# Kernel tuning notes

Hardware: AMD Instinct MI355X
Metric: run time of the kernel (lower is better)

## Reference

```python
import jax, jax.numpy as jnp
import numpy as np

Q_LORA, KV_LORA = 1536, 512
NUM_HEADS, HEAD_DIM = 4, 64
B, QL, KL = 2, 4096, 4096


def setup_inputs() -> dict:
    key = jax.random.key(0)
    k1, k2, k3, k4 = jax.random.split(key, 4)
    q_compressed = jax.random.normal(k1, (B, QL, Q_LORA), dtype=jnp.float32)
    kv_compressed = jax.random.normal(k2, (B, KL, KV_LORA), dtype=jnp.float32)
    # additive causal mask: 0 on/below diagonal, -inf-like above
    causal_mask = jnp.where(
        jnp.arange(QL)[:, None] >= jnp.arange(KL)[None, :], 0.0, -1e9
    ).astype(jnp.float32)
    # learned params (Linear weights stored torch-style as [out, in])
    Wq = 0.01 * jax.random.normal(k3, (NUM_HEADS * HEAD_DIM, Q_LORA), dtype=jnp.float32)
    Wk = 0.01 * jax.random.normal(k4, (NUM_HEADS * HEAD_DIM, KV_LORA), dtype=jnp.float32)
    head_weights = jnp.ones((NUM_HEADS,), dtype=jnp.float32)
    return {
        "q_compressed": q_compressed,
        "kv_compressed": kv_compressed,
        "causal_mask": causal_mask,
        "Wq": Wq,
        "Wk": Wk,
        "head_weights": head_weights,
    }


def reference(q_compressed, kv_compressed, causal_mask, Wq, Wk, head_weights):
    b, ql, _ = q_compressed.shape
    kl = kv_compressed.shape[1]
    # projections: x @ W.T, then split heads
    q_idx = (q_compressed @ Wq.T).reshape(b, ql, NUM_HEADS, HEAD_DIM)  # [b,q,h,d]
    k_idx = (kv_compressed @ Wk.T).reshape(b, kl, NUM_HEADS, HEAD_DIM)  # [b,k,h,d]
    scores = jnp.einsum("bqhd,bkhd->bhqk", q_idx, k_idx)
    scores = jax.nn.relu(scores)
    # head-weighted sum over heads
    index_scores = jnp.einsum("bhqk,h->bqk", scores, head_weights)
    index_scores = index_scores + causal_mask[None, :, :]
    return index_scores
```

## Files before the change

### kernel.cpp

```cpp
#include <hip/hip_runtime.h>
#include <hip/hip_bf16.h>
#include <stdint.h>

typedef __attribute__((ext_vector_type(8))) short bhalf8;
typedef __attribute__((ext_vector_type(4))) float f32x4;
typedef __attribute__((ext_vector_type(4))) unsigned us4;

#define B_ 2
#define QL_ 4096
#define KL_ 4096
#define ND_ 256
#define QLORA_ 1536
#define KVLORA_ 512

__device__ __forceinline__ unsigned pack2(float lo, float hi) {
    union { float f; unsigned u; } a, b; a.f = lo; b.f = hi;
    return __builtin_amdgcn_perm(b.u, a.u, 0x07060302u);
}

__global__ __launch_bounds__(256, 4) void prep_kernel(
    const float* __restrict__ qc, const float* __restrict__ kvc,
    const float* __restrict__ Wq, const float* __restrict__ Wk,
    unsigned short* __restrict__ qidx, unsigned short* __restrict__ kidx)
{
    const int bid = blockIdx.x;
    const int tid = threadIdx.x;

    const float* A; const float* W; unsigned short* C; int K; int pb;
    if (bid < 512) { A = qc;  W = Wq; C = qidx; K = QLORA_;  pb = bid; }
    else           { A = kvc; W = Wk; C = kidx; K = KVLORA_; pb = bid - 512; }

    __shared__ unsigned short sA[2][64][72];
    __shared__ unsigned short sW[2][64][72];

    const int lane = tid & 63;
    const int wid = tid >> 6;

    const int t2 = pb >> 3;
    const int nt = t2 & 3;
    const int mt = (pb & 7) + 8 * (t2 >> 2);
    const int m0 = mt * 64, n0 = nt * 64;

    const int wm = (wid >> 1) * 32;
    const int wn = (wid & 1) * 32;

    const int sr = tid >> 3;
    const int sc = (tid & 7) * 8;

    const float* Abase = A + (size_t)(m0 + sr) * K + sc;
    const float* Wbase = W + (size_t)(n0 + sr) * K + sc;
    const size_t row32 = (size_t)32 * K;

    f32x4 pa[4], pw[4], qa[4], qw[4];
    f32x4 acc[2][2] = {};
    const int nIter = K >> 6;

    auto ISSUE = [&](int kk, f32x4* ra, f32x4* rw) {
        #pragma unroll
        for (int p = 0; p < 2; ++p) {
            ra[2 * p]     = *reinterpret_cast<const f32x4*>(Abase + row32 * p + kk);
            ra[2 * p + 1] = *reinterpret_cast<const f32x4*>(Abase + row32 * p + kk + 4);
            rw[2 * p]     = *reinterpret_cast<const f32x4*>(Wbase + row32 * p + kk);
            rw[2 * p + 1] = *reinterpret_cast<const f32x4*>(Wbase + row32 * p + kk + 4);
        }
    };
    auto WRITE = [&](int buf, f32x4* ra, f32x4* rw) {
        #pragma unroll
        for (int p = 0; p < 2; ++p) {
            us4 va = { pack2(ra[2*p][0], ra[2*p][1]), pack2(ra[2*p][2], ra[2*p][3]),
                       pack2(ra[2*p+1][0], ra[2*p+1][1]), pack2(ra[2*p+1][2], ra[2*p+1][3]) };
            *reinterpret_cast<us4*>(&sA[buf][sr + 32 * p][sc]) = va;
            us4 vw = { pack2(rw[2*p][0], rw[2*p][1]), pack2(rw[2*p][2], rw[2*p][3]),
                       pack2(rw[2*p+1][0], rw[2*p+1][1]), pack2(rw[2*p+1][2], rw[2*p+1][3]) };
            *reinterpret_cast<us4*>(&sW[buf][sr + 32 * p][sc]) = vw;
        }
    };
    auto COMPUTE = [&](int buf) {
        #pragma unroll
        for (int ks = 0; ks < 2; ++ks) {
            const int cb = ks * 32 + (lane >> 4) * 8;
            bhalf8 a0 = *reinterpret_cast<const bhalf8*>(&sA[buf][wm + (lane & 15)][cb]);
            bhalf8 a1 = *reinterpret_cast<const bhalf8*>(&sA[buf][wm + 16 + (lane & 15)][cb]);
            bhalf8 b0 = *reinterpret_cast<const bhalf8*>(&sW[buf][wn + (lane & 15)][cb]);
            bhalf8 b1 = *reinterpret_cast<const bhalf8*>(&sW[buf][wn + 16 + (lane & 15)][cb]);
            acc[0][0] = __builtin_amdgcn_mfma_f32_16x16x32_bf16(a0, b0, acc[0][0], 0, 0, 0);
            acc[0][1] = __builtin_amdgcn_mfma_f32_16x16x32_bf16(a0, b1, acc[0][1], 0, 0, 0);
            acc[1][0] = __builtin_amdgcn_mfma_f32_16x16x32_bf16(a1, b0, acc[1][0], 0, 0, 0);
            acc[1][1] = __builtin_amdgcn_mfma_f32_16x16x32_bf16(a1, b1, acc[1][1], 0, 0, 0);
        }
    };

    ISSUE(0, pa, pw);
    WRITE(0, pa, pw);
    ISSUE(64, pa, pw);
    __syncthreads();

    for (int it = 0; it < nIter; it += 2) {
        if (it + 2 < nIter) ISSUE((it + 2) << 6, qa, qw);
        COMPUTE(0);
        if (it + 1 < nIter) WRITE(1, pa, pw);
        __syncthreads();
        if (it + 3 < nIter) ISSUE((it + 3) << 6, pa, pw);
        COMPUTE(1);
        if (it + 2 < nIter) WRITE(0, qa, qw);
        __syncthreads();
    }

    #pragma unroll
    for (int i = 0; i < 2; ++i) {
        #pragma unroll
        for (int j = 0; j < 2; ++j) {
            int n = n0 + wn + j * 16 + (lane & 15);
            #pragma unroll
            for (int r = 0; r < 4; ++r) {
                int m = m0 + wm + i * 16 + (lane >> 4) * 4 + r;
                union { float f; unsigned u; } x; x.f = acc[i][j][r];
                C[(size_t)m * ND_ + n] = (unsigned short)(x.u >> 16);
            }
        }
    }
}

__global__ __launch_bounds__(512, 2) void scores_kernel(
    const unsigned short* __restrict__ Qi,
    const unsigned short* __restrict__ Ki,
    const float* __restrict__ hw,
    float* __restrict__ out)
{
    const int bx = blockIdx.x;
    const int tid = threadIdx.x;

    if (bx >= 1056) {
        int t = bx - 1056;
        int b = (t >= 496) ? 1 : 0;
        t -= b * 496;
        int tk = (int)((1.0f + __builtin_sqrtf(8.0f * (float)t + 1.0f)) * 0.5f);
        while (tk * (tk - 1) / 2 > t) --tk;
        while (tk * (tk + 1) / 2 <= t) ++tk;
        int tq = t - tk * (tk - 1) / 2;
        float* outb = out + (size_t)b * QL_ * KL_ + (size_t)tq * 128 * KL_ + tk * 128;
        const f32x4 mval = {-1e9f, -1e9f, -1e9f, -1e9f};
        #pragma unroll
        for (int p = 0; p < 8; ++p) {
            int idx = p * 512 + tid;
            int r = idx >> 5;
            int c = (idx & 31) * 4;
            *reinterpret_cast<f32x4*>(&outb[(size_t)r * KL_ + c]) = mval;
        }
        return;
    }

    int g = (bx & 7) * 132 + (bx >> 3);
    int b = (g >= 528) ? 1 : 0;
    int t = g - b * 528;
    int tq = (int)((__builtin_sqrtf(8.0f * (float)t + 1.0f) - 1.0f) * 0.5f);
    while ((tq + 1) * (tq + 2) / 2 <= t) ++tq;
    while (tq * (tq + 1) / 2 > t) --tq;
    int tk = t - tq * (tq + 1) / 2;

    const int q0 = tq * 128, k0 = tk * 128;
    float* outb = out + (size_t)b * QL_ * KL_;

    __shared__ unsigned short sQ[2][128][72];
    __shared__ unsigned short sK[2][128][72];
    const int lane = tid & 63;
    const int wid = tid >> 6;
    const int wq = (wid >> 2) * 64;
    const int wk = (wid & 3) * 32;

    const int hr = tid >> 2;
    const int hc = (tid & 3) * 16;

    float whv[4];
    #pragma unroll
    for (int h = 0; h < 4; ++h) whv[h] = hw[h];

    f32x4 oacc[4][2] = {};
    bhalf8 rq0, rq1, rk0, rk1;

    const unsigned short* Qb = Qi + (size_t)(b * QL_ + q0) * ND_;
    const unsigned short* Kb = Ki + (size_t)(b * KL_ + k0) * ND_;

    auto LOADH = [&](int h) {
        const size_t ro = (size_t)hr * ND_ + h * 64 + hc;
        rq0 = *reinterpret_cast<const bhalf8*>(&Qb[ro]);
        rq1 = *reinterpret_cast<const bhalf8*>(&Qb[ro + 8]);
        rk0 = *reinterpret_cast<const bhalf8*>(&Kb[ro]);
        rk1 = *reinterpret_cast<const bhalf8*>(&Kb[ro + 8]);
    };
    auto WRITEH = [&](int buf) {
        *reinterpret_cast<bhalf8*>(&sQ[buf][hr][hc])     = rq0;
        *reinterpret_cast<bhalf8*>(&sQ[buf][hr][hc + 8]) = rq1;
        *reinterpret_cast<bhalf8*>(&sK[buf][hr][hc])     = rk0;
        *reinterpret_cast<bhalf8*>(&sK[buf][hr][hc + 8]) = rk1;
    };
    auto COMPUTE_H = [&](int buf, int h) {
        f32x4 hacc[4][2] = {};
        #pragma unroll
        for (int ks = 0; ks < 2; ++ks) {
            const int cb = ks * 32 + (lane >> 4) * 8;
            bhalf8 bfr[2];
            #pragma unroll
            for (int j = 0; j < 2; ++j)
                bfr[j] = *reinterpret_cast<const bhalf8*>(&sK[buf][wk + j * 16 + (lane & 15)][cb]);
            #pragma unroll
            for (int i = 0; i < 4; ++i) {
                bhalf8 afr = *reinterpret_cast<const bhalf8*>(&sQ[buf][wq + i * 16 + (lane & 15)][cb]);
                #pragma unroll
                for (int j = 0; j < 2; ++j)
                    hacc[i][j] = __builtin_amdgcn_mfma_f32_16x16x32_bf16(afr, bfr[j], hacc[i][j], 0, 0, 0);
            }
        }
        const float w = whv[h];
        const f32x4 zero = {0.0f, 0.0f, 0.0f, 0.0f};
        #pragma unroll
        for (int i = 0; i < 4; ++i)
            #pragma unroll
            for (int j = 0; j < 2; ++j) {
                f32x4 m = __builtin_elementwise_max(hacc[i][j], zero);
                oacc[i][j] += w * m;
            }
    };

    LOADH(0);
    WRITEH(0);
    __syncthreads();
    #pragma unroll
    for (int h = 0; h < 4; ++h) {
        if (h < 3) LOADH(h + 1);
        COMPUTE_H(h & 1, h);
        if (h < 3) {
            WRITEH((h + 1) & 1);
            __syncthreads();
        }
    }

    const int kcb = k0 + wk + (lane & 15);
    if (tq == tk) {
        #pragma unroll
        for (int i = 0; i < 4; ++i)
            #pragma unroll
            for (int r = 0; r < 4; ++r) {
                int q = q0 + wq + i * 16 + (lane >> 4) * 4 + r;
                #pragma unroll
                for (int j = 0; j < 2; ++j) {
                    int kc = kcb + j * 16;
                    outb[(size_t)q * KL_ + kc] = oacc[i][j][r] + ((kc <= q) ? 0.0f : -1e9f);
                }
            }
    } else {
        #pragma unroll
        for (int i = 0; i < 4; ++i)
            #pragma unroll
            for (int r = 0; r < 4; ++r) {
                int q = q0 + wq + i * 16 + (lane >> 4) * 4 + r;
                #pragma unroll
                for (int j = 0; j < 2; ++j)
                    outb[(size_t)q * KL_ + kcb + j * 16] = oacc[i][j][r];
            }
    }
}

extern "C" void kernel_launch(void* const* d_in, const int* in_sizes, int n_in,
                              void* d_out, int out_size, void* d_ws, size_t ws_size,
                              hipStream_t stream) {
    const float* qc  = (const float*)d_in[0];
    const float* kvc = (const float*)d_in[1];
    const float* Wq  = (const float*)d_in[3];
    const float* Wk  = (const float*)d_in[4];
    const float* hw  = (const float*)d_in[5];

    unsigned short* qidx = (unsigned short*)d_ws;
    unsigned short* kidx = qidx + (size_t)B_ * QL_ * ND_;

    prep_kernel<<<dim3(1024), 256, 0, stream>>>(qc, kvc, Wq, Wk, qidx, kidx);
    scores_kernel<<<dim3(1056 + 992), 512, 0, stream>>>(qidx, kidx, hw, (float*)d_out);
}
```

Baseline: 60.89 us.

## Restructure projection and scores kernels for register-direct fragments and vector stores

The projection kernel now uses 128-row M tiles with half as many blocks. It loads A fragments straight from global memory into registers and converts them to bf16 in place, so only W is staged through LDS. The scores kernel loads all four heads of Q into LDS once and keeps K fragments in registers, removing the per-head syncs. It also swaps MFMA operands so the output can be written as contiguous float4 stores, and raises the occupancy hint. The aim is less LDS traffic, fewer barriers and wider stores, at the cost of uncoalesced direct global fragment loads and higher register pressure.

```diff
diff --git a/kernel.cpp b/kernel.cpp
--- a/kernel.cpp
+++ b/kernel.cpp
@@ -18,7 +18,7 @@
     return __builtin_amdgcn_perm(b.u, a.u, 0x07060302u);
 }
 
-__global__ __launch_bounds__(256, 4) void prep_kernel(
+__global__ __launch_bounds__(256, 2) void prep_kernel(
     const float* __restrict__ qc, const float* __restrict__ kvc,
     const float* __restrict__ Wq, const float* __restrict__ Wk,
     unsigned short* __restrict__ qidx, unsigned short* __restrict__ kidx)
@@ -27,101 +27,105 @@
     const int tid = threadIdx.x;
 
     const float* A; const float* W; unsigned short* C; int K; int pb;
-    if (bid < 512) { A = qc;  W = Wq; C = qidx; K = QLORA_;  pb = bid; }
-    else           { A = kvc; W = Wk; C = kidx; K = KVLORA_; pb = bid - 512; }
-
-    __shared__ unsigned short sA[2][64][72];
+    if (bid < 256) { A = qc;  W = Wq; C = qidx; K = QLORA_;  pb = bid; }
+    else           { A = kvc; W = Wk; C = kidx; K = KVLORA_; pb = bid - 256; }
+
+    const int mt = (pb & 7) + 8 * (pb >> 5);
+    const int nt = (pb >> 3) & 3;
+    const int m0 = mt * 128, n0 = nt * 64;
+
     __shared__ unsigned short sW[2][64][72];
 
     const int lane = tid & 63;
-    const int wid = tid >> 6;
-
-    const int t2 = pb >> 3;
-    const int nt = t2 & 3;
-    const int mt = (pb & 7) + 8 * (t2 >> 2);
-    const int m0 = mt * 64, n0 = nt * 64;
-
-    const int wm = (wid >> 1) * 32;
-    const int wn = (wid & 1) * 32;
-
-    const int sr = tid >> 3;
-    const int sc = (tid & 7) * 8;
-
-    const float* Abase = A + (size_t)(m0 + sr) * K + sc;
-    const float* Wbase = W + (size_t)(n0 + sr) * K + sc;
-    const size_t row32 = (size_t)32 * K;
-
-    f32x4 pa[4], pw[4], qa[4], qw[4];
-    f32x4 acc[2][2] = {};
+    const int w = tid >> 6;
+    const int l15 = lane & 15;
+    const int lh = lane >> 4;
+
+    const float* Arow0 = A + (size_t)(m0 + w * 32 + l15) * K + lh * 8;
+    const float* Arow1 = Arow0 + (size_t)16 * K;
+
+    const int wr = tid >> 2;
+    const int wc = (tid & 3) * 16;
+    const float* Wst = W + (size_t)(n0 + wr) * K + wc;
+
+    f32x4 acc[2][4] = {};
+    f32x4 pa[8], qa[8];
+    f32x4 pw[4], qw[4];
     const int nIter = K >> 6;
 
-    auto ISSUE = [&](int kk, f32x4* ra, f32x4* rw) {
-        #pragma unroll
-        for (int p = 0; p < 2; ++p) {
-            ra[2 * p]     = *reinterpret_cast<const f32x4*>(Abase + row32 * p + kk);
-            ra[2 * p + 1] = *reinterpret_cast<const f32x4*>(Abase + row32 * p + kk + 4);
-            rw[2 * p]     = *reinterpret_cast<const f32x4*>(Wbase + row32 * p + kk);
-            rw[2 * p + 1] = *reinterpret_cast<const f32x4*>(Wbase + row32 * p + kk + 4);
-        }
-    };
-    auto WRITE = [&](int buf, f32x4* ra, f32x4* rw) {
-        #pragma unroll
-        for (int p = 0; p < 2; ++p) {
-            us4 va = { pack2(ra[2*p][0], ra[2*p][1]), pack2(ra[2*p][2], ra[2*p][3]),
-                       pack2(ra[2*p+1][0], ra[2*p+1][1]), pack2(ra[2*p+1][2], ra[2*p+1][3]) };
-            *reinterpret_cast<us4*>(&sA[buf][sr + 32 * p][sc]) = va;
-            us4 vw = { pack2(rw[2*p][0], rw[2*p][1]), pack2(rw[2*p][2], rw[2*p][3]),
-                       pack2(rw[2*p+1][0], rw[2*p+1][1]), pack2(rw[2*p+1][2], rw[2*p+1][3]) };
-            *reinterpret_cast<us4*>(&sW[buf][sr + 32 * p][sc]) = vw;
-        }
-    };
-    auto COMPUTE = [&](int buf) {
+    auto ALOAD = [&](int kk, f32x4* r) {
+        #pragma unroll
+        for (int af = 0; af < 2; ++af) {
+            const float* base = (af ? Arow1 : Arow0) + kk;
+            #pragma unroll
+            for (int ks = 0; ks < 2; ++ks) {
+                r[(af * 2 + ks) * 2 + 0] = *reinterpret_cast<const f32x4*>(base + ks * 32);
+                r[(af * 2 + ks) * 2 + 1] = *reinterpret_cast<const f32x4*>(base + ks * 32 + 4);
+            }
+        }
+    };
+    auto WLOAD = [&](int kk, f32x4* r) {
+        #pragma unroll
+        for (int e = 0; e < 4; ++e)
+            r[e] = *reinterpret_cast<const f32x4*>(Wst + kk + e * 4);
+    };
+    auto WWRITE = [&](int buf, f32x4* r) {
+        us4 v0 = { pack2(r[0][0], r[0][1]), pack2(r[0][2], r[0][3]),
+                   pack2(r[1][0], r[1][1]), pack2(r[1][2], r[1][3]) };
+        us4 v1 = { pack2(r[2][0], r[2][1]), pack2(r[2][2], r[2][3]),
+                   pack2(r[3][0], r[3][1]), pack2(r[3][2], r[3][3]) };
+        *reinterpret_cast<us4*>(&sW[buf][wr][wc])     = v0;
+        *reinterpret_cast<us4*>(&sW[buf][wr][wc + 8]) = v1;
+    };
+    auto COMPUTE = [&](int buf, f32x4* ar) {
         #pragma unroll
         for (int ks = 0; ks < 2; ++ks) {
-            const int cb = ks * 32 + (lane >> 4) * 8;
-            bhalf8 a0 = *reinterpret_cast<const bhalf8*>(&sA[buf][wm + (lane & 15)][cb]);
-            bhalf8 a1 = *reinterpret_cast<const bhalf8*>(&sA[buf][wm + 16 + (lane & 15)][cb]);
-            bhalf8 b0 = *reinterpret_cast<const bhalf8*>(&sW[buf][wn + (lane & 15)][cb]);
-            bhalf8 b1 = *reinterpret_cast<const bhalf8*>(&sW[buf][wn + 16 + (lane & 15)][cb]);
-            acc[0][0] = __builtin_amdgcn_mfma_f32_16x16x32_bf16(a0, b0, acc[0][0], 0, 0, 0);
-            acc[0][1] = __builtin_amdgcn_mfma_f32_16x16x32_bf16(a0, b1, acc[0][1], 0, 0, 0);
-            acc[1][0] = __builtin_amdgcn_mfma_f32_16x16x32_bf16(a1, b0, acc[1][0], 0, 0, 0);
-            acc[1][1] = __builtin_amdgcn_mfma_f32_16x16x32_bf16(a1, b1, acc[1][1], 0, 0, 0);
-        }
-    };
-
-    ISSUE(0, pa, pw);
-    WRITE(0, pa, pw);
-    ISSUE(64, pa, pw);
+            bhalf8 bf[4];
+            #pragma unroll
+            for (int nf = 0; nf < 4; ++nf)
+                bf[nf] = *reinterpret_cast<const bhalf8*>(&sW[buf][nf * 16 + l15][ks * 32 + lh * 8]);
+            #pragma unroll
+            for (int af = 0; af < 2; ++af) {
+                f32x4* r = &ar[(af * 2 + ks) * 2];
+                us4 ap = { pack2(r[0][0], r[0][1]), pack2(r[0][2], r[0][3]),
+                           pack2(r[1][0], r[1][1]), pack2(r[1][2], r[1][3]) };
+                bhalf8 afr = *reinterpret_cast<bhalf8*>(&ap);
+                #pragma unroll
+                for (int nf = 0; nf < 4; ++nf)
+                    acc[af][nf] = __builtin_amdgcn_mfma_f32_16x16x32_bf16(bf[nf], afr, acc[af][nf], 0, 0, 0);
+            }
+        }
+    };
+
+    WLOAD(0, pw); ALOAD(0, pa);
+    WWRITE(0, pw);
     __syncthreads();
 
     for (int it = 0; it < nIter; it += 2) {
-        if (it + 2 < nIter) ISSUE((it + 2) << 6, qa, qw);
-        COMPUTE(0);
-        if (it + 1 < nIter) WRITE(1, pa, pw);
+        WLOAD((it + 1) << 6, qw); ALOAD((it + 1) << 6, qa);
+        COMPUTE(0, pa);
+        WWRITE(1, qw);
         __syncthreads();
-        if (it + 3 < nIter) ISSUE((it + 3) << 6, pa, pw);
-        COMPUTE(1);
-        if (it + 2 < nIter) WRITE(0, qa, qw);
+        if (it + 2 < nIter) { WLOAD((it + 2) << 6, pw); ALOAD((it + 2) << 6, pa); }
+        COMPUTE(1, qa);
+        if (it + 2 < nIter) WWRITE(0, pw);
         __syncthreads();
     }
 
     #pragma unroll
-    for (int i = 0; i < 2; ++i) {
-        #pragma unroll
-        for (int j = 0; j < 2; ++j) {
-            int n = n0 + wn + j * 16 + (lane & 15);
-            #pragma unroll
-            for (int r = 0; r < 4; ++r) {
-                int m = m0 + wm + i * 16 + (lane >> 4) * 4 + r;
-                union { float f; unsigned u; } x; x.f = acc[i][j][r];
-                C[(size_t)m * ND_ + n] = (unsigned short)(x.u >> 16);
-            }
-        }
-    }
-}
-
-__global__ __launch_bounds__(512, 2) void scores_kernel(
+    for (int af = 0; af < 2; ++af) {
+        const size_t mrow = (size_t)(m0 + w * 32 + af * 16 + l15) * ND_;
+        #pragma unroll
+        for (int nf = 0; nf < 4; ++nf) {
+            uint2 v;
+            v.x = pack2(acc[af][nf][0], acc[af][nf][1]);
+            v.y = pack2(acc[af][nf][2], acc[af][nf][3]);
+            *reinterpret_cast<uint2*>(&C[mrow + n0 + nf * 16 + lh * 4]) = v;
+        }
+    }
+}
+
+__global__ __launch_bounds__(512, 4) void scores_kernel(
     const unsigned short* __restrict__ Qi,
     const unsigned short* __restrict__ Ki,
     const float* __restrict__ hw,
@@ -161,103 +165,91 @@
     const int q0 = tq * 128, k0 = tk * 128;
     float* outb = out + (size_t)b * QL_ * KL_;
 
-    __shared__ unsigned short sQ[2][128][72];
-    __shared__ unsigned short sK[2][128][72];
+    __shared__ unsigned short sQ[128][264];
     const int lane = tid & 63;
     const int wid = tid >> 6;
     const int wq = (wid >> 2) * 64;
     const int wk = (wid & 3) * 32;
-
-    const int hr = tid >> 2;
-    const int hc = (tid & 3) * 16;
+    const int l15 = lane & 15;
+    const int lh = lane >> 4;
+
+    const unsigned short* Qb = Qi + (size_t)(b * QL_ + q0) * ND_;
+    const unsigned short* Kb = Ki + (size_t)(b * KL_ + k0) * ND_;
+    const unsigned short* Klane = Kb + (size_t)(wk + l15) * ND_ + lh * 8;
+
+    bhalf8 kfA[4], kfB[4];
+    auto KLOAD = [&](int h, bhalf8* kf) {
+        #pragma unroll
+        for (int j = 0; j < 2; ++j)
+            #pragma unroll
+            for (int ks = 0; ks < 2; ++ks)
+                kf[j * 2 + ks] = *reinterpret_cast<const bhalf8*>(
+                    Klane + (size_t)j * 16 * ND_ + h * 64 + ks * 32);
+    };
+
+    KLOAD(0, kfA);
+
+    {
+        const int qr = tid >> 2;
+        const int qcb = (tid & 3) * 64;
+        #pragma unroll
+        for (int p = 0; p < 8; ++p) {
+            bhalf8 v = *reinterpret_cast<const bhalf8*>(&Qb[(size_t)qr * ND_ + qcb + p * 8]);
+            *reinterpret_cast<bhalf8*>(&sQ[qr][qcb + p * 8]) = v;
+        }
+    }
+    __syncthreads();
 
     float whv[4];
     #pragma unroll
     for (int h = 0; h < 4; ++h) whv[h] = hw[h];
 
-    f32x4 oacc[4][2] = {};
-    bhalf8 rq0, rq1, rk0, rk1;
-
-    const unsigned short* Qb = Qi + (size_t)(b * QL_ + q0) * ND_;
-    const unsigned short* Kb = Ki + (size_t)(b * KL_ + k0) * ND_;
-
-    auto LOADH = [&](int h) {
-        const size_t ro = (size_t)hr * ND_ + h * 64 + hc;
-        rq0 = *reinterpret_cast<const bhalf8*>(&Qb[ro]);
-        rq1 = *reinterpret_cast<const bhalf8*>(&Qb[ro + 8]);
-        rk0 = *reinterpret_cast<const bhalf8*>(&Kb[ro]);
-        rk1 = *reinterpret_cast<const bhalf8*>(&Kb[ro + 8]);
-    };
-    auto WRITEH = [&](int buf) {
-        *reinterpret_cast<bhalf8*>(&sQ[buf][hr][hc])     = rq0;
-        *reinterpret_cast<bhalf8*>(&sQ[buf][hr][hc + 8]) = rq1;
-        *reinterpret_cast<bhalf8*>(&sK[buf][hr][hc])     = rk0;
-        *reinterpret_cast<bhalf8*>(&sK[buf][hr][hc + 8]) = rk1;
-    };
-    auto COMPUTE_H = [&](int buf, int h) {
+    f32x4 acc[4][2] = {};
+
+    auto HEAD = [&](int h, bhalf8* cur, bhalf8* nxt) {
+        if (h < 3) KLOAD(h + 1, nxt);
         f32x4 hacc[4][2] = {};
         #pragma unroll
         for (int ks = 0; ks < 2; ++ks) {
-            const int cb = ks * 32 + (lane >> 4) * 8;
-            bhalf8 bfr[2];
-            #pragma unroll
-            for (int j = 0; j < 2; ++j)
-                bfr[j] = *reinterpret_cast<const bhalf8*>(&sK[buf][wk + j * 16 + (lane & 15)][cb]);
             #pragma unroll
             for (int i = 0; i < 4; ++i) {
-                bhalf8 afr = *reinterpret_cast<const bhalf8*>(&sQ[buf][wq + i * 16 + (lane & 15)][cb]);
-                #pragma unroll
-                for (int j = 0; j < 2; ++j)
-                    hacc[i][j] = __builtin_amdgcn_mfma_f32_16x16x32_bf16(afr, bfr[j], hacc[i][j], 0, 0, 0);
-            }
-        }
-        const float w = whv[h];
+                bhalf8 qf = *reinterpret_cast<const bhalf8*>(
+                    &sQ[wq + i * 16 + l15][h * 64 + ks * 32 + lh * 8]);
+                hacc[i][0] = __builtin_amdgcn_mfma_f32_16x16x32_bf16(cur[0 * 2 + ks], qf, hacc[i][0], 0, 0, 0);
+                hacc[i][1] = __builtin_amdgcn_mfma_f32_16x16x32_bf16(cur[1 * 2 + ks], qf, hacc[i][1], 0, 0, 0);
+            }
+        }
+        const float wgt = whv[h];
         const f32x4 zero = {0.0f, 0.0f, 0.0f, 0.0f};
         #pragma unroll
         for (int i = 0; i < 4; ++i)
             #pragma unroll
             for (int j = 0; j < 2; ++j) {
                 f32x4 m = __builtin_elementwise_max(hacc[i][j], zero);
-                oacc[i][j] += w * m;
-            }
-    };
-
-    LOADH(0);
-    WRITEH(0);
-    __syncthreads();
+                acc[i][j] += wgt * m;
+            }
+    };
+
+    HEAD(0, kfA, kfB);
+    HEAD(1, kfB, kfA);
+    HEAD(2, kfA, kfB);
+    HEAD(3, kfB, kfA);
+
     #pragma unroll
-    for (int h = 0; h < 4; ++h) {
-        if (h < 3) LOADH(h + 1);
-        COMPUTE_H(h & 1, h);
-        if (h < 3) {
-            WRITEH((h + 1) & 1);
-            __syncthreads();
-        }
-    }
-
-    const int kcb = k0 + wk + (lane & 15);
-    if (tq == tk) {
-        #pragma unroll
-        for (int i = 0; i < 4; ++i)
-            #pragma unroll
-            for (int r = 0; r < 4; ++r) {
-                int q = q0 + wq + i * 16 + (lane >> 4) * 4 + r;
+    for (int i = 0; i < 4; ++i) {
+        const int q = q0 + wq + i * 16 + l15;
+        float* rowp = outb + (size_t)q * KL_;
+        #pragma unroll
+        for (int j = 0; j < 2; ++j) {
+            const int kbase = k0 + wk + j * 16 + lh * 4;
+            f32x4 v = acc[i][j];
+            if (tq == tk) {
                 #pragma unroll
-                for (int j = 0; j < 2; ++j) {
-                    int kc = kcb + j * 16;
-                    outb[(size_t)q * KL_ + kc] = oacc[i][j][r] + ((kc <= q) ? 0.0f : -1e9f);
-                }
-            }
-    } else {
-        #pragma unroll
-        for (int i = 0; i < 4; ++i)
-            #pragma unroll
-            for (int r = 0; r < 4; ++r) {
-                int q = q0 + wq + i * 16 + (lane >> 4) * 4 + r;
-                #pragma unroll
-                for (int j = 0; j < 2; ++j)
-                    outb[(size_t)q * KL_ + kcb + j * 16] = oacc[i][j][r];
-            }
+                for (int r = 0; r < 4; ++r)
+                    if (kbase + r > q) v[r] += -1e9f;
+            }
+            *reinterpret_cast<f32x4*>(&rowp[kbase]) = v;
+        }
     }
 }
 
@@ -273,6 +265,6 @@
     unsigned short* qidx = (unsigned short*)d_ws;
     unsigned short* kidx = qidx + (size_t)B_ * QL_ * ND_;
 
-    prep_kernel<<<dim3(1024), 256, 0, stream>>>(qc, kvc, Wq, Wk, qidx, kidx);
+    prep_kernel<<<dim3(512), 256, 0, stream>>>(qc, kvc, Wq, Wk, qidx, kidx);
     scores_kernel<<<dim3(1056 + 992), 512, 0, stream>>>(qidx, kidx, hw, (float*)d_out);
 }
```

Result: slower. 112.3 us (+84.4%).

## Transpose MFMA operands for vector stores, interleave fill blocks, use nontemporal writes

Applied to the files above, without the earlier changes.

Swaps the MFMA A/B operands so each lane holds four consecutive key columns of one query row. The epilogue can then emit 16-byte vector stores instead of scalar stores. Output stores, including the masked-tile fill, use nontemporal hints to avoid polluting cache with the write-only 128MB output. Block indices are remapped so compute and mask-fill blocks are interleaved in groups of 8, spreading pure-store work across the run instead of leaving it all at the tail.

```diff
diff --git a/kernel.cpp b/kernel.cpp
--- a/kernel.cpp
+++ b/kernel.cpp
@@ -16,6 +16,10 @@
 __device__ __forceinline__ unsigned pack2(float lo, float hi) {
     union { float f; unsigned u; } a, b; a.f = lo; b.f = hi;
     return __builtin_amdgcn_perm(b.u, a.u, 0x07060302u);
+}
+
+__device__ __forceinline__ void nt_store4(float* p, f32x4 v) {
+    __builtin_nontemporal_store(v, reinterpret_cast<f32x4*>(p));
 }
 
 __global__ __launch_bounds__(256, 4) void prep_kernel(
@@ -130,10 +134,18 @@
     const int bx = blockIdx.x;
     const int tid = threadIdx.x;
 
-    if (bx >= 1056) {
-        int t = bx - 1056;
-        int b = (t >= 496) ? 1 : 0;
-        t -= b * 496;
+    int c = -1, f = -1;
+    if (bx < 1984) {
+        const int seg = bx >> 4, w = bx & 15;
+        if (w < 8) c = seg * 8 + w;
+        else       f = seg * 8 + (w - 8);
+    } else {
+        c = 992 + (bx - 1984);
+    }
+
+    if (f >= 0) {
+        int b = (f >= 496) ? 1 : 0;
+        int t = f - b * 496;
         int tk = (int)((1.0f + __builtin_sqrtf(8.0f * (float)t + 1.0f)) * 0.5f);
         while (tk * (tk - 1) / 2 > t) --tk;
         while (tk * (tk + 1) / 2 <= t) ++tk;
@@ -144,13 +156,13 @@
         for (int p = 0; p < 8; ++p) {
             int idx = p * 512 + tid;
             int r = idx >> 5;
-            int c = (idx & 31) * 4;
-            *reinterpret_cast<f32x4*>(&outb[(size_t)r * KL_ + c]) = mval;
+            int cc = (idx & 31) * 4;
+            nt_store4(&outb[(size_t)r * KL_ + cc], mval);
         }
         return;
     }
 
-    int g = (bx & 7) * 132 + (bx >> 3);
+    int g = (c & 7) * 132 + (c >> 3);
     int b = (g >= 528) ? 1 : 0;
     int t = g - b * 528;
     int tq = (int)((__builtin_sqrtf(8.0f * (float)t + 1.0f) - 1.0f) * 0.5f);
@@ -167,6 +179,8 @@
     const int wid = tid >> 6;
     const int wq = (wid >> 2) * 64;
     const int wk = (wid & 3) * 32;
+    const int l15 = lane & 15;
+    const int lh = lane >> 4;
 
     const int hr = tid >> 2;
     const int hc = (tid & 3) * 16;
@@ -175,7 +189,7 @@
     #pragma unroll
     for (int h = 0; h < 4; ++h) whv[h] = hw[h];
 
-    f32x4 oacc[4][2] = {};
+    f32x4 acc[4][2] = {};
     bhalf8 rq0, rq1, rk0, rk1;
 
     const unsigned short* Qb = Qi + (size_t)(b * QL_ + q0) * ND_;
@@ -198,27 +212,27 @@
         f32x4 hacc[4][2] = {};
         #pragma unroll
         for (int ks = 0; ks < 2; ++ks) {
-            const int cb = ks * 32 + (lane >> 4) * 8;
-            bhalf8 bfr[2];
+            const int cb = ks * 32 + lh * 8;
+            bhalf8 kfr[2];
             #pragma unroll
             for (int j = 0; j < 2; ++j)
-                bfr[j] = *reinterpret_cast<const bhalf8*>(&sK[buf][wk + j * 16 + (lane & 15)][cb]);
+                kfr[j] = *reinterpret_cast<const bhalf8*>(&sK[buf][wk + j * 16 + l15][cb]);
             #pragma unroll
             for (int i = 0; i < 4; ++i) {
-                bhalf8 afr = *reinterpret_cast<const bhalf8*>(&sQ[buf][wq + i * 16 + (lane & 15)][cb]);
+                bhalf8 qfr = *reinterpret_cast<const bhalf8*>(&sQ[buf][wq + i * 16 + l15][cb]);
                 #pragma unroll
                 for (int j = 0; j < 2; ++j)
-                    hacc[i][j] = __builtin_amdgcn_mfma_f32_16x16x32_bf16(afr, bfr[j], hacc[i][j], 0, 0, 0);
-            }
-        }
-        const float w = whv[h];
+                    hacc[i][j] = __builtin_amdgcn_mfma_f32_16x16x32_bf16(kfr[j], qfr, hacc[i][j], 0, 0, 0);
+            }
+        }
+        const float wgt = whv[h];
         const f32x4 zero = {0.0f, 0.0f, 0.0f, 0.0f};
         #pragma unroll
         for (int i = 0; i < 4; ++i)
             #pragma unroll
             for (int j = 0; j < 2; ++j) {
                 f32x4 m = __builtin_elementwise_max(hacc[i][j], zero);
-                oacc[i][j] += w * m;
+                acc[i][j] += wgt * m;
             }
     };
 
@@ -235,29 +249,21 @@
         }
     }
 
-    const int kcb = k0 + wk + (lane & 15);
-    if (tq == tk) {
-        #pragma unroll
-        for (int i = 0; i < 4; ++i)
-            #pragma unroll
-            for (int r = 0; r < 4; ++r) {
-                int q = q0 + wq + i * 16 + (lane >> 4) * 4 + r;
+    #pragma unroll
+    for (int i = 0; i < 4; ++i) {
+        const int q = q0 + wq + i * 16 + l15;
+        float* rowp = outb + (size_t)q * KL_;
+        #pragma unroll
+        for (int j = 0; j < 2; ++j) {
+            const int kbase = k0 + wk + j * 16 + lh * 4;
+            f32x4 v = acc[i][j];
+            if (tq == tk) {
                 #pragma unroll
-                for (int j = 0; j < 2; ++j) {
-                    int kc = kcb + j * 16;
-                    outb[(size_t)q * KL_ + kc] = oacc[i][j][r] + ((kc <= q) ? 0.0f : -1e9f);
-                }
-            }
-    } else {
-        #pragma unroll
-        for (int i = 0; i < 4; ++i)
-            #pragma unroll
-            for (int r = 0; r < 4; ++r) {
-                int q = q0 + wq + i * 16 + (lane >> 4) * 4 + r;
-                #pragma unroll
-                for (int j = 0; j < 2; ++j)
-                    outb[(size_t)q * KL_ + kcb + j * 16] = oacc[i][j][r];
-            }
+                for (int r = 0; r < 4; ++r)
+                    if (kbase + r > q) v[r] += -1e9f;
+            }
+            nt_store4(&rowp[kbase], v);
+        }
     }
 }
 
@@ -274,5 +280,5 @@
     unsigned short* kidx = qidx + (size_t)B_ * QL_ * ND_;
 
     prep_kernel<<<dim3(1024), 256, 0, stream>>>(qc, kvc, Wq, Wk, qidx, kidx);
-    scores_kernel<<<dim3(1056 + 992), 512, 0, stream>>>(qidx, kidx, hw, (float*)d_out);
-}
+    scores_kernel<<<dim3(2048), 512, 0, stream>>>(qidx, kidx, hw, (float*)d_out);
+}
```

Result: slower. 75.28 us (+23.6%).

## Load MFMA operands directly from global memory, dropping LDS staging

Applied to the files above, without the earlier changes.

The scores kernel no longer stages Q and K head tiles through double-buffered shared memory with barriers. Each lane now loads its MFMA fragments straight from global memory, and launch bounds are raised to allow more resident blocks. This removes LDS traffic and __syncthreads, but each Q/K element is now fetched redundantly by several waves through the cache hierarchy, with no software prefetch overlap.

```diff
diff --git a/kernel.cpp b/kernel.cpp
--- a/kernel.cpp
+++ b/kernel.cpp
@@ -121,7 +121,7 @@
     }
 }
 
-__global__ __launch_bounds__(512, 2) void scores_kernel(
+__global__ __launch_bounds__(512, 4) void scores_kernel(
     const unsigned short* __restrict__ Qi,
     const unsigned short* __restrict__ Ki,
     const float* __restrict__ hw,
@@ -161,91 +161,64 @@
     const int q0 = tq * 128, k0 = tk * 128;
     float* outb = out + (size_t)b * QL_ * KL_;
 
-    __shared__ unsigned short sQ[2][128][72];
-    __shared__ unsigned short sK[2][128][72];
     const int lane = tid & 63;
     const int wid = tid >> 6;
     const int wq = (wid >> 2) * 64;
     const int wk = (wid & 3) * 32;
-
-    const int hr = tid >> 2;
-    const int hc = (tid & 3) * 16;
+    const int l15 = lane & 15;
+    const int lh = lane >> 4;
+
+    const unsigned short* Qlane = Qi + (size_t)(b * QL_ + q0 + wq + l15) * ND_ + lh * 8;
+    const unsigned short* Klane = Ki + (size_t)(b * KL_ + k0 + wk + l15) * ND_ + lh * 8;
 
     float whv[4];
     #pragma unroll
     for (int h = 0; h < 4; ++h) whv[h] = hw[h];
 
-    f32x4 oacc[4][2] = {};
-    bhalf8 rq0, rq1, rk0, rk1;
-
-    const unsigned short* Qb = Qi + (size_t)(b * QL_ + q0) * ND_;
-    const unsigned short* Kb = Ki + (size_t)(b * KL_ + k0) * ND_;
-
-    auto LOADH = [&](int h) {
-        const size_t ro = (size_t)hr * ND_ + h * 64 + hc;
-        rq0 = *reinterpret_cast<const bhalf8*>(&Qb[ro]);
-        rq1 = *reinterpret_cast<const bhalf8*>(&Qb[ro + 8]);
-        rk0 = *reinterpret_cast<const bhalf8*>(&Kb[ro]);
-        rk1 = *reinterpret_cast<const bhalf8*>(&Kb[ro + 8]);
-    };
-    auto WRITEH = [&](int buf) {
-        *reinterpret_cast<bhalf8*>(&sQ[buf][hr][hc])     = rq0;
-        *reinterpret_cast<bhalf8*>(&sQ[buf][hr][hc + 8]) = rq1;
-        *reinterpret_cast<bhalf8*>(&sK[buf][hr][hc])     = rk0;
-        *reinterpret_cast<bhalf8*>(&sK[buf][hr][hc + 8]) = rk1;
-    };
-    auto COMPUTE_H = [&](int buf, int h) {
-        f32x4 hacc[4][2] = {};
-        #pragma unroll
-        for (int ks = 0; ks < 2; ++ks) {
-            const int cb = ks * 32 + (lane >> 4) * 8;
-            bhalf8 bfr[2];
-            #pragma unroll
-            for (int j = 0; j < 2; ++j)
-                bfr[j] = *reinterpret_cast<const bhalf8*>(&sK[buf][wk + j * 16 + (lane & 15)][cb]);
-            #pragma unroll
-            for (int i = 0; i < 4; ++i) {
-                bhalf8 afr = *reinterpret_cast<const bhalf8*>(&sQ[buf][wq + i * 16 + (lane & 15)][cb]);
-                #pragma unroll
-                for (int j = 0; j < 2; ++j)
-                    hacc[i][j] = __builtin_amdgcn_mfma_f32_16x16x32_bf16(afr, bfr[j], hacc[i][j], 0, 0, 0);
-            }
-        }
-        const float w = whv[h];
-        const f32x4 zero = {0.0f, 0.0f, 0.0f, 0.0f};
-        #pragma unroll
-        for (int i = 0; i < 4; ++i)
-            #pragma unroll
-            for (int j = 0; j < 2; ++j) {
-                f32x4 m = __builtin_elementwise_max(hacc[i][j], zero);
-                oacc[i][j] += w * m;
-            }
-    };
-
-    LOADH(0);
-    WRITEH(0);
-    __syncthreads();
+    f32x4 acc[4][2] = {};
+    const f32x4 zero = {0.0f, 0.0f, 0.0f, 0.0f};
+
     #pragma unroll
     for (int h = 0; h < 4; ++h) {
-        if (h < 3) LOADH(h + 1);
-        COMPUTE_H(h & 1, h);
-        if (h < 3) {
-            WRITEH((h + 1) & 1);
-            __syncthreads();
-        }
-    }
-
-    const int kcb = k0 + wk + (lane & 15);
+        bhalf8 qf[4][2], kf[2][2];
+        #pragma unroll
+        for (int i = 0; i < 4; ++i)
+            #pragma unroll
+            for (int ks = 0; ks < 2; ++ks)
+                qf[i][ks] = *reinterpret_cast<const bhalf8*>(
+                    Qlane + (size_t)i * 16 * ND_ + h * 64 + ks * 32);
+        #pragma unroll
+        for (int j = 0; j < 2; ++j)
+            #pragma unroll
+            for (int ks = 0; ks < 2; ++ks)
+                kf[j][ks] = *reinterpret_cast<const bhalf8*>(
+                    Klane + (size_t)j * 16 * ND_ + h * 64 + ks * 32);
+
+        const float wgt = whv[h];
+        #pragma unroll
+        for (int i = 0; i < 4; ++i) {
+            #pragma unroll
+            for (int j = 0; j < 2; ++j) {
+                f32x4 hacc = zero;
+                hacc = __builtin_amdgcn_mfma_f32_16x16x32_bf16(qf[i][0], kf[j][0], hacc, 0, 0, 0);
+                hacc = __builtin_amdgcn_mfma_f32_16x16x32_bf16(qf[i][1], kf[j][1], hacc, 0, 0, 0);
+                f32x4 m = __builtin_elementwise_max(hacc, zero);
+                acc[i][j] += wgt * m;
+            }
+        }
+    }
+
+    const int kcb = k0 + wk + l15;
     if (tq == tk) {
         #pragma unroll
         for (int i = 0; i < 4; ++i)
             #pragma unroll
             for (int r = 0; r < 4; ++r) {
-                int q = q0 + wq + i * 16 + (lane >> 4) * 4 + r;
+                int q = q0 + wq + i * 16 + lh * 4 + r;
                 #pragma unroll
                 for (int j = 0; j < 2; ++j) {
                     int kc = kcb + j * 16;
-                    outb[(size_t)q * KL_ + kc] = oacc[i][j][r] + ((kc <= q) ? 0.0f : -1e9f);
+                    outb[(size_t)q * KL_ + kc] = acc[i][j][r] + ((kc <= q) ? 0.0f : -1e9f);
                 }
             }
     } else {
@@ -253,10 +226,10 @@
         for (int i = 0; i < 4; ++i)
             #pragma unroll
             for (int r = 0; r < 4; ++r) {
-                int q = q0 + wq + i * 16 + (lane >> 4) * 4 + r;
+                int q = q0 + wq + i * 16 + lh * 4 + r;
                 #pragma unroll
                 for (int j = 0; j < 2; ++j)
-                    outb[(size_t)q * KL_ + kcb + j * 16] = oacc[i][j][r];
+                    outb[(size_t)q * KL_ + kcb + j * 16] = acc[i][j][r];
             }
     }
 }
```

New measurement: 90.95 us. 49.4% more time.
